# Optimization experiments

Hardware: AMD Instinct MI355X
Metric: run time of the kernel (lower is better)

The kernel has to match this reference:

```python
import jax, jax.numpy as jnp
import numpy as np

B, P, M, C = 8, 131072, 16, 2
THRESHOLD = 0.5
GAMMA = 2.0
ALPHA_W = 0.25  # focal 'weight' for the foreground class


def _cxcycz_to_xyz(b):
    return jnp.concatenate([b[..., :3] - b[..., 3:] / 2, b[..., :3] + b[..., 3:] / 2], -1)


def _xyz_to_cxcycz(b):
    return jnp.concatenate([(b[..., :3] + b[..., 3:]) / 2, b[..., 3:] - b[..., :3]], -1)


def _encode(cxcycz, priors_cxcycz):
    # standard SSD encoding with variances (10, 5), extended to 3D
    return jnp.concatenate([
        (cxcycz[..., :3] - priors_cxcycz[..., :3]) / (priors_cxcycz[..., 3:] / 10.0),
        jnp.log(cxcycz[..., 3:] / priors_cxcycz[..., 3:]) * 5.0], -1)


def _jaccard3d(a, b):
    # a: [M,6] xyz boxes, b: [P,6] xyz boxes -> [M,P] IoU
    lo = jnp.maximum(a[:, None, :3], b[None, :, :3])
    hi = jnp.minimum(a[:, None, 3:], b[None, :, 3:])
    inter = jnp.prod(jnp.clip(hi - lo, 0.0, None), -1)
    va = jnp.prod(a[:, 3:] - a[:, :3], -1)
    vb = jnp.prod(b[:, 3:] - b[:, :3], -1)
    return inter / (va[:, None] + vb[None, :] - inter)


def setup_inputs():
    key = jax.random.key(0)
    k1, k2, k3, k4, k5, k6 = jax.random.split(key, 6)
    predicted_locs = jax.random.normal(k1, (B, P, 6), jnp.float32)
    predicted_scores = jax.random.normal(k2, (B, P, C), jnp.float32)
    # valid ground-truth boxes in boundary (xyz) coords inside unit cube
    ctr = jax.random.uniform(k3, (B, M, 3)) * 0.8 + 0.1
    sz = jax.random.uniform(k4, (B, M, 3)) * 0.15 + 0.05
    boxes = jnp.concatenate([ctr - sz / 2, ctr + sz / 2], -1)
    # priors in center-size (cxcycz) coords
    pctr = jax.random.uniform(k5, (P, 3)) * 0.9 + 0.05
    psz = jax.random.uniform(k6, (P, 3)) * 0.2 + 0.03
    priors_cxcycz = jnp.concatenate([pctr, psz], -1)
    labels = jnp.ones((B, M), jnp.int32)  # single foreground class
    return dict(predicted_locs=predicted_locs, predicted_scores=predicted_scores,
                boxes=boxes, labels=labels, priors_cxcycz=priors_cxcycz)


def _forward(predicted_locs, predicted_scores, boxes, priors_cxcycz, labels):
    priors_xyz = _cxcycz_to_xyz(priors_cxcycz)

    def match(boxes_i, labels_i):
        ov = _jaccard3d(boxes_i, priors_xyz)           # [M, P]
        overlap_fep = ov.max(0)                        # [P] best IoU per prior
        object_fep = ov.argmax(0)                      # [P] best object per prior
        prior_feo = ov.argmax(1)                       # [M] best prior per object
        # force each object to own its best prior
        object_fep = object_fep.at[prior_feo].set(jnp.arange(M))
        overlap_fep = overlap_fep.at[prior_feo].set(1.0)
        lab = labels_i[object_fep]
        lab = jnp.where(overlap_fep < THRESHOLD, 0, lab)  # hard thresholding
        tl = _encode(_xyz_to_cxcycz(boxes_i[object_fep]), priors_cxcycz)
        return lab, tl

    true_classes, true_locs = jax.vmap(match)(boxes, labels)  # [B,P], [B,P,6]

    pos = true_classes > 0
    n_pos = pos.sum()
    # nn.L1Loss() = mean over all selected elements (n_pos priors x 6 coords)
    diff = jnp.abs(predicted_locs - true_locs) * pos[..., None].astype(predicted_locs.dtype)
    loc_loss = jnp.where(n_pos > 0,
                         diff.sum() / jnp.maximum(n_pos.astype(jnp.float32) * 6.0, 1.0),
                         jnp.float32(0.0))

    # sigmoid focal loss on foreground channel (include_background=False, C==2)
    x = predicted_scores[..., 1]                       # [B,P] fg logit
    t = pos.astype(x.dtype)
    ce = -(t * jax.nn.log_sigmoid(x) + (1.0 - t) * jax.nn.log_sigmoid(-x))
    p = jax.nn.sigmoid(x)
    pt = jnp.where(pos, p, 1.0 - p)
    focal = (ALPHA_W * t + (1.0 - ALPHA_W) * (1.0 - t)) * (1.0 - pt) ** GAMMA * ce
    conf_loss = focal.mean()
    return conf_loss, loc_loss


def reference(predicted_locs, predicted_scores, boxes, labels, priors_cxcycz):
    return _forward(predicted_locs, predicted_scores, boxes, priors_cxcycz, labels)
```

## Files before the change

### kernel.cpp

```cpp
#include <hip/hip_runtime.h>

#define NB 8
#define NP 131072
#define NM 16
#define THRESH 0.5f
#define BLK 256
#define BPB (NP / BLK)
#define MATCH_BLOCKS (NB * BPB)
#define FOCAL_BLOCKS 128
#define NBLOCKS (MATCH_BLOCKS + FOCAL_BLOCKS)
#define NPAIR (NB * NM)

typedef unsigned long long u64;
typedef unsigned int u32;


template <int CTRL>
__device__ __forceinline__ float dppmv(float x) {
    return __int_as_float(__builtin_amdgcn_update_dpp(
        0, __float_as_int(x), CTRL, 0xf, 0xf, false));
}

__device__ __forceinline__ float wave_max63(float x) {
    x = fmaxf(x, dppmv<0x111>(x));
    x = fmaxf(x, dppmv<0x112>(x));
    x = fmaxf(x, dppmv<0x114>(x));
    x = fmaxf(x, dppmv<0x118>(x));
    x = fmaxf(x, dppmv<0x142>(x));
    x = fmaxf(x, dppmv<0x143>(x));
    return x;
}

__device__ __forceinline__ float wave_sum63(float x) {
    x += dppmv<0x111>(x);
    x += dppmv<0x112>(x);
    x += dppmv<0x114>(x);
    x += dppmv<0x118>(x);
    x += dppmv<0x142>(x);
    x += dppmv<0x143>(x);
    return x;
}

__device__ __forceinline__ float bcast63(float x) {
    return __int_as_float(__builtin_amdgcn_readlane(__float_as_int(x), 63));
}


__device__ __forceinline__ float iou_term(float inter, float va, float vb) {
    return (inter > 0.0f) ? inter * __builtin_amdgcn_rcpf(va + vb - inter) : 0.0f;
}

__device__ __forceinline__ float focal_term(float x, bool pos) {
    float t = __expf(-fabsf(x));
    float r = __builtin_amdgcn_rcpf(1.0f + t);
    float L = __logf(1.0f + t);
    float ce = (pos ? fmaxf(-x, 0.0f) : fmaxf(x, 0.0f)) + L;
    float omp = (pos == (x >= 0.0f)) ? t * r : r;
    float w = pos ? 0.25f : 0.75f;
    return w * omp * omp * ce;
}

__device__ __forceinline__ float l1_enc(const float* lp,
                                        const float blo[3], const float bhi[3],
                                        const float pc[3], const float ps[3]) {
    float s = 0.0f;
#pragma unroll
    for (int k = 0; k < 3; ++k) {
        float gc = (blo[k] + bhi[k]) / 2.0f;
        float gs = bhi[k] - blo[k];
        float e  = (gc - pc[k]) / (ps[k] / 10.0f);
        float e2 = __logf(gs / ps[k]) * 5.0f;
        s += fabsf(lp[k]     - e);
        s += fabsf(lp[3 + k] - e2);
    }
    return s;
}

__device__ __forceinline__ u32 decode_p(u64 k) { return ~(u32)(k & 0xFFFFFFFFull); }


__global__ __launch_bounds__(BLK) void main_kernel(
        const float* __restrict__ locs, const float* __restrict__ scores,
        const float* __restrict__ boxes, const int* __restrict__ labels,
        const float* __restrict__ priors,
        u64* __restrict__ keys_out,
        float4* __restrict__ part) {
    __shared__ float4 s_box[NM][2];
    __shared__ u64    s_wkey[4][NM];
    __shared__ float  s_wred[4][3];

    const int tid  = threadIdx.x;
    const int bid  = blockIdx.x;
    const int lane = tid & 63, wave = tid >> 6;

    if (bid >= MATCH_BLOCKS) {
        const int fblk = bid - MATCH_BLOCKS;
        const float4* sc4 = reinterpret_cast<const float4*>(scores);
        float f = 0.0f;
#pragma unroll
        for (int i = 0; i < 16; ++i) {
            float4 v = sc4[(size_t)fblk * 4096 + i * BLK + tid];
            f += focal_term(v.y, false) + focal_term(v.w, false);
        }
        f = wave_sum63(f);
        if (lane == 63) s_wred[wave][0] = f;
        __syncthreads();
        if (tid == 0)
            part[bid] = make_float4(s_wred[0][0] + s_wred[1][0] +
                                    s_wred[2][0] + s_wred[3][0], 0.0f, 0.0f, 0.0f);
        return;
    }

    const int b    = bid >> 9;
    const int xblk = bid & (BPB - 1);
    const int p    = (xblk << 8) | tid;
    const int pbase = (xblk << 8) | (wave << 6);

    if (tid < NM) {
        const float* bx = &boxes[(b * NM + tid) * 6];
        float l0 = bx[0], l1 = bx[1], l2 = bx[2];
        float h0 = bx[3], h1 = bx[4], h2 = bx[5];
        s_box[tid][0] = make_float4(l0, l1, l2, h0);
        float va = (h0 - l0) * (h1 - l1) * (h2 - l2);
        s_box[tid][1] = make_float4(h1, h2, va, __int_as_float(labels[b * NM + tid]));
    }
    __syncthreads();

    const float2* pr2 = reinterpret_cast<const float2*>(priors);
    float2 q0 = pr2[(size_t)p * 3 + 0], q1 = pr2[(size_t)p * 3 + 1], q2 = pr2[(size_t)p * 3 + 2];
    float pl[3], ph[3];
    {
        const float pcf[3] = {q0.x, q0.y, q1.x};
        const float psf[3] = {q1.y, q2.x, q2.y};
#pragma unroll
        for (int k = 0; k < 3; ++k) {
            pl[k] = pcf[k] - psf[k] / 2.0f;
            ph[k] = pcf[k] + psf[k] / 2.0f;
        }
    }
    const float vb = (ph[0] - pl[0]) * (ph[1] - pl[1]) * (ph[2] - pl[2]);

    float best = -1.0f; int bm = 0;
#pragma unroll
    for (int m = 0; m < NM; ++m) {
        float4 A = s_box[m][0], B4 = s_box[m][1];
        float d0 = fminf(A.w,  ph[0]) - fmaxf(A.x, pl[0]);
        float d1 = fminf(B4.x, ph[1]) - fmaxf(A.y, pl[1]);
        float d2 = fminf(B4.y, ph[2]) - fmaxf(A.z, pl[2]);
        float inter = fmaxf(d0, 0.0f) * fmaxf(d1, 0.0f) * fmaxf(d2, 0.0f);
        float iou = iou_term(inter, B4.z, vb);
        if (iou > best) { best = iou; bm = m; }
        float wm = bcast63(wave_max63(iou));
        u64 eq = __ballot(iou == wm);
        int ls = __ffsll(eq) - 1;
        if (lane == 0)
            s_wkey[wave][m] = ((u64)__float_as_uint(wm) << 32)
                            | (u32)~(u32)(pbase + ls);
    }

    float4 Bb = s_box[bm][1];
    const bool pos = (best >= THRESH) && (__float_as_int(Bb.w) > 0);
    float f = 0.0f, l = 0.0f, n = 0.0f;
    if (pos) {
        const float x = scores[((size_t)b * NP + p) * 2 + 1];
        f = focal_term(x, true) - focal_term(x, false);
        float4 Ab = s_box[bm][0];
        float blo[3] = {Ab.x, Ab.y, Ab.z}, bhi[3] = {Ab.w, Bb.x, Bb.y};
        const float pcr[3] = {q0.x, q0.y, q1.x};
        const float psr[3] = {q1.y, q2.x, q2.y};
        l = l1_enc(&locs[((size_t)b * NP + p) * 6], blo, bhi, pcr, psr);
        n = 1.0f;
    }

    f = wave_sum63(f); l = wave_sum63(l); n = wave_sum63(n);
    if (lane == 63) { s_wred[wave][0] = f; s_wred[wave][1] = l; s_wred[wave][2] = n; }
    __syncthreads();

    if (tid < NM) {
        u64 k = s_wkey[0][tid];
#pragma unroll
        for (int w = 1; w < 4; ++w) k = (s_wkey[w][tid] > k) ? s_wkey[w][tid] : k;
        keys_out[(size_t)(b * NM + tid) * BPB + xblk] = k;
    }
    if (tid == 0) {
        part[bid] = make_float4(s_wred[0][0] + s_wred[1][0] + s_wred[2][0] + s_wred[3][0],
                                s_wred[0][1] + s_wred[1][1] + s_wred[2][1] + s_wred[3][1],
                                s_wred[0][2] + s_wred[1][2] + s_wred[2][2] + s_wred[3][2],
                                0.0f);
    }
}


__global__ __launch_bounds__(1024) void finalize_kernel(
        const float* __restrict__ locs, const float* __restrict__ scores,
        const float* __restrict__ boxes, const int* __restrict__ labels,
        const float* __restrict__ priors, const u64* __restrict__ keys_in,
        const float4* __restrict__ part, float* __restrict__ out) {
    __shared__ u64   s_key[NPAIR];
    __shared__ float s_red[16][3];
    __shared__ float s_fix[16][3];
    const int t = threadIdx.x, lane = t & 63, wave = t >> 6;

    float f = 0.0f, l = 0.0f, n = 0.0f;
    for (int i = t; i < NBLOCKS; i += 1024) {
        float4 v = part[i]; f += v.x; l += v.y; n += v.z;
    }
    f = wave_sum63(f); l = wave_sum63(l); n = wave_sum63(n);
    if (lane == 63) { s_red[wave][0] = f; s_red[wave][1] = l; s_red[wave][2] = n; }

#pragma unroll
    for (int i = 0; i < 8; ++i) {
        const int pair = wave * 8 + i;
        const u64* kp = keys_in + (size_t)pair * BPB;
        u64 k = 0;
#pragma unroll
        for (int j = 0; j < BPB / 64; ++j) {
            u64 v = kp[j * 64 + lane];
            k = (v > k) ? v : k;
        }
#pragma unroll
        for (int off = 32; off > 0; off >>= 1) {
            u64 o = __shfl_down(k, off);
            k = (o > k) ? o : k;
        }
        if (lane == 0) s_key[pair] = k;
    }
    __syncthreads();

    float df = 0.0f, dl = 0.0f, dn = 0.0f;
    if (t < NPAIR) {
        const int b = t / NM, m = t % NM;
        const u32 pstar = decode_p(s_key[t]);
        bool skip = false;
        for (int mm = m + 1; mm < NM; ++mm)
            skip |= (decode_p(s_key[b * NM + mm]) == pstar);
        if (!skip) {
            const int p = (int)pstar;
            float pc[3], ps[3], pl[3], ph[3];
#pragma unroll
            for (int k = 0; k < 3; ++k) { pc[k] = priors[p * 6 + k]; ps[k] = priors[p * 6 + 3 + k]; }
#pragma unroll
            for (int k = 0; k < 3; ++k) { pl[k] = pc[k] - ps[k] / 2.0f; ph[k] = pc[k] + ps[k] / 2.0f; }
            const float vb = (ph[0] - pl[0]) * (ph[1] - pl[1]) * (ph[2] - pl[2]);

            float best = -1.0f; int bestm = 0;
            for (int mm = 0; mm < NM; ++mm) {
                const float* bx = &boxes[(b * NM + mm) * 6];
                float d0 = fminf(bx[3], ph[0]) - fmaxf(bx[0], pl[0]);
                float d1 = fminf(bx[4], ph[1]) - fmaxf(bx[1], pl[1]);
                float d2 = fminf(bx[5], ph[2]) - fmaxf(bx[2], pl[2]);
                float inter = fmaxf(d0, 0.0f) * fmaxf(d1, 0.0f) * fmaxf(d2, 0.0f);
                float va = (bx[3] - bx[0]) * (bx[4] - bx[1]) * (bx[5] - bx[2]);
                float iou = iou_term(inter, va, vb);
                if (iou > best) { best = iou; bestm = mm; }
            }
            const bool old_pos = (best >= THRESH) && (labels[b * NM + bestm] > 0);
            const bool new_pos = (labels[b * NM + m] > 0);

            const float x = scores[((size_t)b * NP + p) * 2 + 1];
            df = focal_term(x, new_pos) - focal_term(x, old_pos);
            dn = (new_pos ? 1.0f : 0.0f) - (old_pos ? 1.0f : 0.0f);

            const float* lp = &locs[((size_t)b * NP + p) * 6];
            if (new_pos) {
                const float* bx = &boxes[(b * NM + m) * 6];
                float blo[3] = {bx[0], bx[1], bx[2]}, bhi[3] = {bx[3], bx[4], bx[5]};
                dl += l1_enc(lp, blo, bhi, pc, ps);
            }
            if (old_pos) {
                const float* bx = &boxes[(b * NM + bestm) * 6];
                float blo[3] = {bx[0], bx[1], bx[2]}, bhi[3] = {bx[3], bx[4], bx[5]};
                dl -= l1_enc(lp, blo, bhi, pc, ps);
            }
        }
    }
    df = wave_sum63(df); dl = wave_sum63(dl); dn = wave_sum63(dn);
    if (lane == 63) { s_fix[wave][0] = df; s_fix[wave][1] = dl; s_fix[wave][2] = dn; }
    __syncthreads();

    if (t == 0) {
        float tf = 0.0f, tl = 0.0f, tn = 0.0f;
        for (int w = 0; w < 16; ++w) {
            tf += s_red[w][0] + s_fix[w][0];
            tl += s_red[w][1] + s_fix[w][1];
            tn += s_red[w][2] + s_fix[w][2];
        }
        out[0] = tf / (float)(NB * NP);
        out[1] = (tn > 0.5f) ? tl / fmaxf(tn * 6.0f, 1.0f) : 0.0f;
    }
}


extern "C" void kernel_launch(void* const* d_in, const int* in_sizes, int n_in,
                              void* d_out, int out_size, void* d_ws, size_t ws_size,
                              hipStream_t stream) {
    const float* locs   = (const float*)d_in[0];
    const float* scores = (const float*)d_in[1];
    const float* boxes  = (const float*)d_in[2];
    const int*   labels = (const int*)d_in[3];
    const float* priors = (const float*)d_in[4];
    float* out = (float*)d_out;

    u64*    keys = (u64*)d_ws;
    float4* part = (float4*)((char*)d_ws + (size_t)NPAIR * BPB * 8);

    main_kernel<<<NBLOCKS, BLK, 0, stream>>>(locs, scores, boxes, labels, priors,
                                             keys, part);
    finalize_kernel<<<1, 1024, 0, stream>>>(locs, scores, boxes, labels, priors, keys,
                                            part, out);
}
```

Before: 42.92 us.

## Replace per-wave DPP argmax reduction with filtered LDS 64-bit atomicMax keys

Each thread now builds a packed (IoU, inverted prior index) key per ground-truth box. It issues an LDS atomicMax only when its key beats the current shared value. This replaces the per-box wave max, ballot and cross-wave merge. Each shared key is seeded with the block's lowest-index zero-IoU key, so most threads skip the atomic. Focal-only blocks now come first in the grid, and prior centres and sizes are reloaded from global memory in the positive path, which frees registers. The risk is atomic contention when many lanes see nonzero IoU for the same box.

```diff
diff --git a/kernel.cpp b/kernel.cpp
--- a/kernel.cpp
+++ b/kernel.cpp
@@ -21,16 +21,6 @@
         0, __float_as_int(x), CTRL, 0xf, 0xf, false));
 }
 
-__device__ __forceinline__ float wave_max63(float x) {
-    x = fmaxf(x, dppmv<0x111>(x));
-    x = fmaxf(x, dppmv<0x112>(x));
-    x = fmaxf(x, dppmv<0x114>(x));
-    x = fmaxf(x, dppmv<0x118>(x));
-    x = fmaxf(x, dppmv<0x142>(x));
-    x = fmaxf(x, dppmv<0x143>(x));
-    return x;
-}
-
 __device__ __forceinline__ float wave_sum63(float x) {
     x += dppmv<0x111>(x);
     x += dppmv<0x112>(x);
@@ -41,10 +31,6 @@
     return x;
 }
 
-__device__ __forceinline__ float bcast63(float x) {
-    return __int_as_float(__builtin_amdgcn_readlane(__float_as_int(x), 63));
-}
-
 
 __device__ __forceinline__ float iou_term(float inter, float va, float vb) {
     return (inter > 0.0f) ? inter * __builtin_amdgcn_rcpf(va + vb - inter) : 0.0f;
@@ -86,20 +72,18 @@
         u64* __restrict__ keys_out,
         float4* __restrict__ part) {
     __shared__ float4 s_box[NM][2];
-    __shared__ u64    s_wkey[4][NM];
+    __shared__ u64    s_key[NM];
     __shared__ float  s_wred[4][3];
 
     const int tid  = threadIdx.x;
     const int bid  = blockIdx.x;
     const int lane = tid & 63, wave = tid >> 6;
 
-    if (bid >= MATCH_BLOCKS) {
-        const int fblk = bid - MATCH_BLOCKS;
+    if (bid < FOCAL_BLOCKS) {
         const float4* sc4 = reinterpret_cast<const float4*>(scores);
         float f = 0.0f;
-#pragma unroll
         for (int i = 0; i < 16; ++i) {
-            float4 v = sc4[(size_t)fblk * 4096 + i * BLK + tid];
+            float4 v = sc4[(size_t)bid * 4096 + i * BLK + tid];
             f += focal_term(v.y, false) + focal_term(v.w, false);
         }
         f = wave_sum63(f);
@@ -111,10 +95,10 @@
         return;
     }
 
-    const int b    = bid >> 9;
-    const int xblk = bid & (BPB - 1);
+    const int mbid = bid - FOCAL_BLOCKS;
+    const int b    = mbid >> 9;
+    const int xblk = mbid & (BPB - 1);
     const int p    = (xblk << 8) | tid;
-    const int pbase = (xblk << 8) | (wave << 6);
 
     if (tid < NM) {
         const float* bx = &boxes[(b * NM + tid) * 6];
@@ -123,6 +107,7 @@
         s_box[tid][0] = make_float4(l0, l1, l2, h0);
         float va = (h0 - l0) * (h1 - l1) * (h2 - l2);
         s_box[tid][1] = make_float4(h1, h2, va, __int_as_float(labels[b * NM + tid]));
+        s_key[tid] = (u64)(u32)~(u32)(xblk << 8);
     }
     __syncthreads();
 
@@ -139,6 +124,7 @@
         }
     }
     const float vb = (ph[0] - pl[0]) * (ph[1] - pl[1]) * (ph[2] - pl[2]);
+    const u32 pinv = ~(u32)p;
 
     float best = -1.0f; int bm = 0;
 #pragma unroll
@@ -150,12 +136,9 @@
         float inter = fmaxf(d0, 0.0f) * fmaxf(d1, 0.0f) * fmaxf(d2, 0.0f);
         float iou = iou_term(inter, B4.z, vb);
         if (iou > best) { best = iou; bm = m; }
-        float wm = bcast63(wave_max63(iou));
-        u64 eq = __ballot(iou == wm);
-        int ls = __ffsll(eq) - 1;
-        if (lane == 0)
-            s_wkey[wave][m] = ((u64)__float_as_uint(wm) << 32)
-                            | (u32)~(u32)(pbase + ls);
+        u64 key = ((u64)__float_as_uint(iou) << 32) | pinv;
+        if (key > s_key[m])
+            atomicMax(&s_key[m], key);
     }
 
     float4 Bb = s_box[bm][1];
@@ -166,9 +149,10 @@
         f = focal_term(x, true) - focal_term(x, false);
         float4 Ab = s_box[bm][0];
         float blo[3] = {Ab.x, Ab.y, Ab.z}, bhi[3] = {Ab.w, Bb.x, Bb.y};
-        const float pcr[3] = {q0.x, q0.y, q1.x};
-        const float psr[3] = {q1.y, q2.x, q2.y};
-        l = l1_enc(&locs[((size_t)b * NP + p) * 6], blo, bhi, pcr, psr);
+        float pc[3], ps[3];
+#pragma unroll
+        for (int k = 0; k < 3; ++k) { pc[k] = priors[p * 6 + k]; ps[k] = priors[p * 6 + 3 + k]; }
+        l = l1_enc(&locs[((size_t)b * NP + p) * 6], blo, bhi, pc, ps);
         n = 1.0f;
     }
 
@@ -176,12 +160,8 @@
     if (lane == 63) { s_wred[wave][0] = f; s_wred[wave][1] = l; s_wred[wave][2] = n; }
     __syncthreads();
 
-    if (tid < NM) {
-        u64 k = s_wkey[0][tid];
-#pragma unroll
-        for (int w = 1; w < 4; ++w) k = (s_wkey[w][tid] > k) ? s_wkey[w][tid] : k;
-        keys_out[(size_t)(b * NM + tid) * BPB + xblk] = k;
-    }
+    if (tid < NM)
+        keys_out[(size_t)(b * NM + tid) * BPB + xblk] = s_key[tid];
     if (tid == 0) {
         part[bid] = make_float4(s_wred[0][0] + s_wred[1][0] + s_wred[2][0] + s_wred[3][0],
                                 s_wred[0][1] + s_wred[1][1] + s_wred[2][1] + s_wred[3][1],
```

Result: faster. 39.94 us (-6.9%).
